# Optimization experiments

Hardware: AMD Instinct MI355X
Metric: run time of the kernel (lower is better)

The kernel has to match this reference:

```python
import jax, jax.numpy as jnp
import numpy as np
import math

B, L, H, NH = 8, 512, 512, 8
DH = H // NH


def setup_inputs() -> dict:
    key = jax.random.key(0)
    ks = jax.random.split(key, 12)
    src = jax.random.normal(ks[0], (B, L, H), dtype=jnp.float32)
    seq_len = jax.random.randint(ks[1], (B,), L // 2, L + 1).astype(jnp.int32)
    seq_len = seq_len.at[0].set(L)  # guarantee max(seq_len) == L
    pe = jax.random.normal(ks[2], (2 * L, H), dtype=jnp.float32) * 0.02
    s = 1.0 / math.sqrt(H)
    Wq = jax.random.normal(ks[3], (H, H), dtype=jnp.float32) * s
    bq = jnp.zeros((H,), jnp.float32)
    Wk = jax.random.normal(ks[4], (H, H), dtype=jnp.float32) * s
    bk = jnp.zeros((H,), jnp.float32)
    Wv = jax.random.normal(ks[5], (H, H), dtype=jnp.float32) * s
    bv = jnp.zeros((H,), jnp.float32)
    Wr = jax.random.normal(ks[6], (H, H), dtype=jnp.float32) * s
    br = jnp.zeros((H,), jnp.float32)
    u = jax.random.normal(ks[7], (NH, DH), dtype=jnp.float32) * 0.02
    v = jax.random.normal(ks[8], (NH, DH), dtype=jnp.float32) * 0.02
    gamma = jnp.ones((H,), jnp.float32)
    beta = jnp.zeros((H,), jnp.float32)
    return dict(src=src, seq_len=seq_len, pe=pe, Wq=Wq, bq=bq, Wk=Wk, bk=bk,
                Wv=Wv, bv=bv, Wr=Wr, br=br, u=u, v=v, gamma=gamma, beta=beta)


def reference(src, seq_len, pe, Wq, bq, Wk, bk, Wv, bv, Wr, br, u, v, gamma, beta):
    b, l, h = src.shape
    dh = h // NH
    # relative distance rel[i,j] = j - i, lookup pe[rel + L]  -> [L, L, H]
    rel = jnp.arange(l)[None, :] - jnp.arange(l)[:, None]
    R = pe[rel + l]
    # projections (torch Linear: y = x W^T + b)
    q = src @ Wq.T + bq
    k = src @ Wk.T + bk
    val = src @ Wv.T + bv
    R = R @ Wr.T + br
    # split heads
    q = q.reshape(b, l, NH, dh)
    k = k.reshape(b, l, NH, dh)
    val = val.reshape(b, l, NH, dh)
    R = R.reshape(l, l, NH, dh)
    # Transformer-XL score terms
    A = jnp.einsum('bihd,bjhd->bhij', q, k)
    Bt = jnp.einsum('bihd,ijhd->bhij', q, R)
    C = jnp.einsum('hd,bjhd->bhj', u, k)[:, :, None, :]
    D = jnp.einsum('ijhd,hd->hij', R, v)[None]
    scores = (A + Bt + C + D) / math.sqrt(dh)
    # key-side padding mask
    mask = jnp.arange(l)[None, :] < seq_len[:, None]  # [B, L]
    scores = jnp.where(mask[:, None, None, :], scores, jnp.float32(-1e15))
    attn = jax.nn.softmax(scores, axis=-1)
    out = jnp.einsum('bhij,bjhd->bihd', attn, val).reshape(b, l, h)
    res = src + out
    # LayerNorm (eps=1e-5) then exact GELU
    mu = jnp.mean(res, axis=-1, keepdims=True)
    var = jnp.mean((res - mu) ** 2, axis=-1, keepdims=True)
    ln = (res - mu) * jax.lax.rsqrt(var + 1e-5) * gamma + beta
    return jax.nn.gelu(ln, approximate=False)
```

## Files before the change

### kernel.cpp

```cpp
#include <hip/hip_runtime.h>
#include <math.h>

#define Bn 8
#define Ln 512
#define Hn 512
#define NHn 8
#define DHn 64

typedef __attribute__((ext_vector_type(8))) short short8;
typedef __attribute__((ext_vector_type(4))) float f32x4;

__device__ __forceinline__ unsigned short f2bf(float f) {
    unsigned int u = __float_as_uint(f);
    unsigned int r = (u + 0x7FFFu + ((u >> 16) & 1u)) >> 16;
    return (unsigned short)r;
}
__device__ __forceinline__ float bf2f(unsigned short s) {
    return __uint_as_float(((unsigned int)s) << 16);
}

__global__ __launch_bounds__(256) void convert_kernel(
    const float* __restrict__ src, const float* __restrict__ pe,
    const float* __restrict__ Wq, const float* __restrict__ Wk,
    const float* __restrict__ Wv, const float* __restrict__ Wr,
    const float* __restrict__ bq, const float* __restrict__ bk,
    const float* __restrict__ bv,
    unsigned short* __restrict__ src_bf, unsigned short* __restrict__ pe_bf,
    unsigned short* __restrict__ Wcat_bf, unsigned short* __restrict__ Wr_bf,
    float* __restrict__ bcat)
{
    const int bid = blockIdx.x;
    const int tid = threadIdx.x;
    const float* in; unsigned short* outp; int base4;
    if (bid < 2048)      { in = src; outp = src_bf;           base4 = bid; }
    else if (bid < 2560) { in = pe;  outp = pe_bf;            base4 = bid - 2048; }
    else if (bid < 2816) { in = Wq;  outp = Wcat_bf;          base4 = bid - 2560; }
    else if (bid < 3072) { in = Wk;  outp = Wcat_bf + 262144; base4 = bid - 2816; }
    else if (bid < 3328) { in = Wv;  outp = Wcat_bf + 524288; base4 = bid - 3072; }
    else if (bid < 3584) { in = Wr;  outp = Wr_bf;            base4 = bid - 3328; }
    else {
        const int idx = (bid - 3584) * 256 + tid;
        if (idx < 512)            bcat[idx] = bq[idx];
        else if (idx < 1024)      bcat[idx] = bk[idx - 512];
        else if (idx < 1536)      bcat[idx] = bv[idx - 1024];
        return;
    }
    const int i4 = (base4 * 256 + tid) * 4;
    float4 x = *(const float4*)&in[i4];
    ushort4 o;
    o.x = f2bf(x.x); o.y = f2bf(x.y); o.z = f2bf(x.z); o.w = f2bf(x.w);
    *(ushort4*)&outp[i4] = o;
}

__global__ __launch_bounds__(256) void gemm_kernel(
    const unsigned short* __restrict__ src_bf,
    const unsigned short* __restrict__ Wcat_bf,
    const unsigned short* __restrict__ pe_bf,
    const unsigned short* __restrict__ Wr_bf,
    const float* __restrict__ bcat, const float* __restrict__ br,
    unsigned short* __restrict__ QKb,
    unsigned short* __restrict__ VTg,
    unsigned short* __restrict__ Rpb)
{
    const int bid = blockIdx.x;
    int mode, m0, n0;
    const unsigned short *A, *B;
    if (bid < 256) {
        mode = 0; n0 = (bid & 7) * 128; m0 = (bid >> 3) * 128;
        A = src_bf + (size_t)m0 * 512;
        B = Wcat_bf + (size_t)n0 * 512;
    } else if (bid < 384) {
        mode = 1; m0 = ((bid - 256) & 3) * 128; n0 = ((bid - 256) >> 2) * 128;
        A = Wcat_bf + (size_t)(1024 + m0) * 512;
        B = src_bf + (size_t)n0 * 512;
    } else {
        mode = 2; n0 = ((bid - 384) & 3) * 128; m0 = ((bid - 384) >> 2) * 128;
        A = pe_bf + (size_t)m0 * 512;
        B = Wr_bf + (size_t)n0 * 512;
    }

    __shared__ unsigned short As[128 * 32];
    __shared__ unsigned short Bs[128 * 32];

    const int t = threadIdx.x;
    const int wave = t >> 6, lane = t & 63;
    const int wm = (wave >> 1) * 64;
    const int wn = (wave & 1) * 64;

    f32x4 acc[4][4] = {};

    const int srow = wave * 32 + (lane >> 2);
    const int scol = (lane & 3) * 8;
    const unsigned short* Ag = A + (size_t)srow * 512 + scol;
    const unsigned short* Bg = B + (size_t)srow * 512 + scol;
    unsigned short* AsW = &As[srow * 32 + scol];
    unsigned short* BsW = &Bs[srow * 32 + scol];

    uint4 a0 = *(const uint4*)(Ag);
    uint4 a1 = *(const uint4*)(Ag + 16 * 512);
    uint4 b0 = *(const uint4*)(Bg);
    uint4 b1 = *(const uint4*)(Bg + 16 * 512);

    for (int k0 = 0; k0 < 512; k0 += 32) {
        __syncthreads();
        *(uint4*)(AsW)           = a0;
        *(uint4*)(AsW + 16 * 32) = a1;
        *(uint4*)(BsW)           = b0;
        *(uint4*)(BsW + 16 * 32) = b1;
        __syncthreads();

        if (k0 + 32 < 512) {
            a0 = *(const uint4*)(Ag + k0 + 32);
            a1 = *(const uint4*)(Ag + k0 + 32 + 16 * 512);
            b0 = *(const uint4*)(Bg + k0 + 32);
            b1 = *(const uint4*)(Bg + k0 + 32 + 16 * 512);
        }

        short8 af[4], bf[4];
        #pragma unroll
        for (int mt = 0; mt < 4; ++mt)
            af[mt] = *(const short8*)&As[(wm + mt * 16 + (lane & 15)) * 32 + (lane >> 4) * 8];
        #pragma unroll
        for (int nt = 0; nt < 4; ++nt)
            bf[nt] = *(const short8*)&Bs[(wn + nt * 16 + (lane & 15)) * 32 + (lane >> 4) * 8];
        #pragma unroll
        for (int mt = 0; mt < 4; ++mt)
            #pragma unroll
            for (int nt = 0; nt < 4; ++nt)
                acc[mt][nt] = __builtin_amdgcn_mfma_f32_16x16x32_bf16(
                    af[mt], bf[nt], acc[mt][nt], 0, 0, 0);
    }

    const int crow = (lane >> 4) * 4;
    const int ccol = lane & 15;
    if (mode == 0) {
        #pragma unroll
        for (int mt = 0; mt < 4; ++mt)
            #pragma unroll
            for (int nt = 0; nt < 4; ++nt) {
                const int n = n0 + wn + nt * 16 + ccol;
                const float bn = bcat[n];
                #pragma unroll
                for (int r = 0; r < 4; ++r) {
                    const int m = m0 + wm + mt * 16 + crow + r;
                    QKb[(size_t)m * 1024 + n] = f2bf(acc[mt][nt][r] + bn);
                }
            }
    } else if (mode == 1) {
        #pragma unroll
        for (int mt = 0; mt < 4; ++mt)
            #pragma unroll
            for (int nt = 0; nt < 4; ++nt) {
                const int n = n0 + wn + nt * 16 + ccol;
                #pragma unroll
                for (int r = 0; r < 4; ++r) {
                    const int dv = m0 + wm + mt * 16 + crow + r;
                    VTg[(size_t)dv * 4096 + n] = f2bf(acc[mt][nt][r] + bcat[1024 + dv]);
                }
            }
    } else {
        #pragma unroll
        for (int mt = 0; mt < 4; ++mt)
            #pragma unroll
            for (int nt = 0; nt < 4; ++nt) {
                const int n = n0 + wn + nt * 16 + ccol;
                const float bn = br[n];
                #pragma unroll
                for (int r = 0; r < 4; ++r) {
                    const int m = m0 + wm + mt * 16 + crow + r;
                    Rpb[(size_t)m * 512 + n] = f2bf(acc[mt][nt][r] + bn);
                }
            }
    }
}

#define PADK 72
__global__ __launch_bounds__(256) void attn_kernel(
    const unsigned short* __restrict__ QKb,
    const unsigned short* __restrict__ VTg,
    const unsigned short* __restrict__ Rpb,
    const float* __restrict__ u, const float* __restrict__ v,
    const int* __restrict__ seq_len, unsigned short* __restrict__ Ob)
{
    const int i0 = blockIdx.x * 64;
    const int h  = blockIdx.y;
    const int b  = blockIdx.z;
    const int slen = seq_len[b];
    const int njt = (slen + 63) >> 6;

    __shared__ unsigned short k_s [64 * PADK];
    __shared__ unsigned short vT_s[64 * PADK];
    __shared__ unsigned short rs_s[64 * PADK];
    __shared__ unsigned short p_s [64 * PADK];
    __shared__ unsigned short qrTT[128 * 72];

    const int t = threadIdx.x;
    const int wave = t >> 6, lane = t & 63;
    const int l = lane & 15, g = lane >> 4;

    short8 af_qu[2], af_qv[2];
    {
        const unsigned short* qrow =
            QKb + (size_t)(b * 512 + i0 + wave * 16 + l) * 1024 + h * 64;
        #pragma unroll
        for (int kk = 0; kk < 2; ++kk) {
            const int c = kk * 32 + g * 8;
            unsigned short q8[8];
            *(uint4*)q8 = *(const uint4*)(qrow + c);
            float4 u0 = *(const float4*)(u + h * 64 + c);
            float4 u1 = *(const float4*)(u + h * 64 + c + 4);
            float4 v0 = *(const float4*)(v + h * 64 + c);
            float4 v1 = *(const float4*)(v + h * 64 + c + 4);
            float uf[8] = {u0.x,u0.y,u0.z,u0.w,u1.x,u1.y,u1.z,u1.w};
            float vf[8] = {v0.x,v0.y,v0.z,v0.w,v1.x,v1.y,v1.z,v1.w};
            short8 qu, qv;
            #pragma unroll
            for (int e = 0; e < 8; ++e) {
                float qf = bf2f(q8[e]);
                qu[e] = (short)f2bf(qf + uf[e]);
                qv[e] = (short)f2bf(qf + vf[e]);
            }
            af_qu[kk] = qu; af_qv[kk] = qv;
        }
    }

    float m_run[4], l_run[4];
    f32x4 accO[4] = {};
    #pragma unroll
    for (int r = 0; r < 4; ++r) { m_run[r] = -3.0e38f; l_run[r] = 0.f; }

    const int jr = t >> 2, c0 = (t & 3) * 16;

    auto btChunk = [&](int slot0) {
        #pragma unroll
        for (int nt8 = 0; nt8 < 4; ++nt8) {
            f32x4 a = {};
            #pragma unroll
            for (int kk = 0; kk < 2; ++kk) {
                short8 br8 = *(const short8*)&rs_s[(nt8 * 16 + l) * PADK + kk * 32 + g * 8];
                a = __builtin_amdgcn_mfma_f32_16x16x32_bf16(af_qv[kk], br8, a, 0, 0, 0);
            }
            const int sl = slot0 + nt8 * 16 + l;
            ushort4 w4;
            w4.x = f2bf(a[0]); w4.y = f2bf(a[1]); w4.z = f2bf(a[2]); w4.w = f2bf(a[3]);
            *(ushort4*)(qrTT + sl * 72 + wave * 16 + g * 4) = w4;
        }
    };

    const unsigned short* rpA = Rpb + (size_t)(448 - i0 + jr) * 512 + h * 64 + c0;
    uint4 rA0 = *(const uint4*)(rpA);
    uint4 rA1 = *(const uint4*)(rpA + 8);
    const unsigned short* kp0 = QKb + (size_t)(b * 512 + jr) * 1024 + 512 + h * 64 + c0;
    uint4 kc0 = *(const uint4*)(kp0), kc1 = *(const uint4*)(kp0 + 8);
    const unsigned short* vp0 = VTg + (size_t)(h * 64 + jr) * 4096 + b * 512 + c0;
    uint4 vc0 = *(const uint4*)(vp0), vc1 = *(const uint4*)(vp0 + 8);
    const unsigned short* rp0 = Rpb + (size_t)(512 - i0 + jr) * 512 + h * 64 + c0;
    uint4 rc0 = *(const uint4*)(rp0), rc1 = *(const uint4*)(rp0 + 8);

    *(uint4*)(rs_s + jr * PADK + c0)     = rA0;
    *(uint4*)(rs_s + jr * PADK + c0 + 8) = rA1;
    __syncthreads();
    btChunk((448 - i0) & 127);

    for (int jt = 0; jt < njt; ++jt) {
        const int j0 = jt * 64;
        __syncthreads();

        *(uint4*)(k_s  + jr * PADK + c0)     = kc0;
        *(uint4*)(k_s  + jr * PADK + c0 + 8) = kc1;
        *(uint4*)(vT_s + jr * PADK + c0)     = vc0;
        *(uint4*)(vT_s + jr * PADK + c0 + 8) = vc1;
        *(uint4*)(rs_s + jr * PADK + c0)     = rc0;
        *(uint4*)(rs_s + jr * PADK + c0 + 8) = rc1;
        __syncthreads();

        if (jt + 1 < njt) {
            const unsigned short* kp =
                QKb + (size_t)(b * 512 + j0 + 64 + jr) * 1024 + 512 + h * 64 + c0;
            kc0 = *(const uint4*)(kp); kc1 = *(const uint4*)(kp + 8);
            const unsigned short* vp =
                VTg + (size_t)(h * 64 + jr) * 4096 + b * 512 + j0 + 64 + c0;
            vc0 = *(const uint4*)(vp); vc1 = *(const uint4*)(vp + 8);
            const unsigned short* rp =
                Rpb + (size_t)(j0 + 64 - i0 + 512 + jr) * 512 + h * 64 + c0;
            rc0 = *(const uint4*)(rp); rc1 = *(const uint4*)(rp + 8);
        }

        btChunk((j0 - i0 + 512) & 127);

        f32x4 accA[4];
        #pragma unroll
        for (int nt = 0; nt < 4; ++nt) {
            f32x4 a = {};
            #pragma unroll
            for (int kk = 0; kk < 2; ++kk) {
                short8 bk8 = *(const short8*)&k_s[(nt * 16 + l) * PADK + kk * 32 + g * 8];
                a = __builtin_amdgcn_mfma_f32_16x16x32_bf16(af_qu[kk], bk8, a, 0, 0, 0);
            }
            accA[nt] = a;
        }

        float sv[4][4];
        #pragma unroll
        for (int nt = 0; nt < 4; ++nt)
            #pragma unroll
            for (int r = 0; r < 4; ++r) {
                const int il = wave * 16 + g * 4 + r;
                const int slot = (j0 + nt * 16 + l - i0 - il + 512) & 127;
                const float qr = bf2f(qrTT[slot * 72 + il]);
                float s = (accA[nt][r] + qr) * 0.125f;
                if (j0 + nt * 16 + l >= slen) s = -1e15f;
                sv[nt][r] = s;
            }

        float alpha_r[4];
        #pragma unroll
        for (int r = 0; r < 4; ++r) {
            float tm = fmaxf(fmaxf(sv[0][r], sv[1][r]), fmaxf(sv[2][r], sv[3][r]));
            tm = fmaxf(tm, __shfl_xor(tm, 1, 64));
            tm = fmaxf(tm, __shfl_xor(tm, 2, 64));
            tm = fmaxf(tm, __shfl_xor(tm, 4, 64));
            tm = fmaxf(tm, __shfl_xor(tm, 8, 64));
            const float mn = fmaxf(m_run[r], tm);
            alpha_r[r] = __expf(m_run[r] - mn);
            m_run[r] = mn;
            float ss = 0.f;
            #pragma unroll
            for (int nt = 0; nt < 4; ++nt) {
                const float pe_ = __expf(sv[nt][r] - mn);
                sv[nt][r] = pe_; ss += pe_;
            }
            ss += __shfl_xor(ss, 1, 64);
            ss += __shfl_xor(ss, 2, 64);
            ss += __shfl_xor(ss, 4, 64);
            ss += __shfl_xor(ss, 8, 64);
            l_run[r] = l_run[r] * alpha_r[r] + ss;
        }

        #pragma unroll
        for (int nt = 0; nt < 4; ++nt)
            #pragma unroll
            for (int r = 0; r < 4; ++r)
                p_s[(wave * 16 + g * 4 + r) * PADK + nt * 16 + l] = f2bf(sv[nt][r]);

        #pragma unroll
        for (int nt = 0; nt < 4; ++nt)
            #pragma unroll
            for (int r = 0; r < 4; ++r)
                accO[nt][r] *= alpha_r[r];

        short8 pa[2];
        #pragma unroll
        for (int kk = 0; kk < 2; ++kk)
            pa[kk] = *(const short8*)&p_s[(wave * 16 + l) * PADK + kk * 32 + g * 8];
        #pragma unroll
        for (int nt = 0; nt < 4; ++nt) {
            #pragma unroll
            for (int kk = 0; kk < 2; ++kk) {
                short8 bv8 = *(const short8*)&vT_s[(nt * 16 + l) * PADK + kk * 32 + g * 8];
                accO[nt] = __builtin_amdgcn_mfma_f32_16x16x32_bf16(pa[kk], bv8, accO[nt], 0, 0, 0);
            }
        }
    }

    float inv[4];
    #pragma unroll
    for (int r = 0; r < 4; ++r) inv[r] = 1.0f / l_run[r];
    #pragma unroll
    for (int nt = 0; nt < 4; ++nt)
        #pragma unroll
        for (int r = 0; r < 4; ++r)
            Ob[(size_t)(b * 512 + i0 + wave * 16 + g * 4 + r) * 512 + h * 64 + nt * 16 + l]
                = f2bf(accO[nt][r] * inv[r]);
}

__global__ __launch_bounds__(256) void ln_gelu_kernel(
    const float* __restrict__ src, const unsigned short* __restrict__ Ob,
    const float* __restrict__ gamma, const float* __restrict__ beta,
    float* __restrict__ out)
{
    const int row  = blockIdx.x * 4 + (threadIdx.x >> 6);
    const int lane = threadIdx.x & 63;
    const int c0   = lane * 8;
    const float* s = &src[(size_t)row * 512 + c0];
    float4 s0 = *(const float4*)(s);
    float4 s1 = *(const float4*)(s + 4);
    unsigned short o8[8];
    *(uint4*)o8 = *(const uint4*)(Ob + (size_t)row * 512 + c0);
    float x[8];
    x[0] = s0.x + bf2f(o8[0]); x[1] = s0.y + bf2f(o8[1]);
    x[2] = s0.z + bf2f(o8[2]); x[3] = s0.w + bf2f(o8[3]);
    x[4] = s1.x + bf2f(o8[4]); x[5] = s1.y + bf2f(o8[5]);
    x[6] = s1.z + bf2f(o8[6]); x[7] = s1.w + bf2f(o8[7]);
    float sum = 0.f;
    #pragma unroll
    for (int e = 0; e < 8; ++e) sum += x[e];
    #pragma unroll
    for (int off = 32; off >= 1; off >>= 1) sum += __shfl_xor(sum, off, 64);
    const float mean = sum * (1.0f / 512.0f);
    float var = 0.f;
    #pragma unroll
    for (int e = 0; e < 8; ++e) { float d = x[e] - mean; var += d * d; }
    #pragma unroll
    for (int off = 32; off >= 1; off >>= 1) var += __shfl_xor(var, off, 64);
    var *= (1.0f / 512.0f);
    const float inv = rsqrtf(var + 1e-5f);
    float4 g0 = *(const float4*)(gamma + c0);
    float4 g1 = *(const float4*)(gamma + c0 + 4);
    float4 b0 = *(const float4*)(beta + c0);
    float4 b1 = *(const float4*)(beta + c0 + 4);
    float gm[8] = {g0.x,g0.y,g0.z,g0.w,g1.x,g1.y,g1.z,g1.w};
    float bt[8] = {b0.x,b0.y,b0.z,b0.w,b1.x,b1.y,b1.z,b1.w};
    float r8[8];
    #pragma unroll
    for (int e = 0; e < 8; ++e) {
        float ln = (x[e] - mean) * inv * gm[e] + bt[e];
        r8[e] = 0.5f * ln * (1.0f + erff(ln * 0.70710678118654752f));
    }
    float* op = &out[(size_t)row * 512 + c0];
    *(float4*)(op)     = make_float4(r8[0], r8[1], r8[2], r8[3]);
    *(float4*)(op + 4) = make_float4(r8[4], r8[5], r8[6], r8[7]);
}

extern "C" void kernel_launch(void* const* d_in, const int* in_sizes, int n_in,
                              void* d_out, int out_size, void* d_ws, size_t ws_size,
                              hipStream_t stream)
{
    const float* src     = (const float*)d_in[0];
    const int*   seq_len = (const int*)  d_in[1];
    const float* pe      = (const float*)d_in[2];
    const float* Wq      = (const float*)d_in[3];
    const float* bq      = (const float*)d_in[4];
    const float* Wk      = (const float*)d_in[5];
    const float* bk      = (const float*)d_in[6];
    const float* Wv      = (const float*)d_in[7];
    const float* bv      = (const float*)d_in[8];
    const float* Wr      = (const float*)d_in[9];
    const float* br      = (const float*)d_in[10];
    const float* u       = (const float*)d_in[11];
    const float* v       = (const float*)d_in[12];
    const float* gamma   = (const float*)d_in[13];
    const float* beta    = (const float*)d_in[14];
    float* out = (float*)d_out;

    char* w = (char*)d_ws;
    unsigned short* QKb     = (unsigned short*)(w);
    unsigned short* VTg     = (unsigned short*)(w + 8388608);
    unsigned short* Rpb     = (unsigned short*)(w + 12582912);
    unsigned short* Ob      = (unsigned short*)(w + 13631488);
    unsigned short* src_bf  = (unsigned short*)(w + 17825792);
    unsigned short* pe_bf   = (unsigned short*)(w + 22020096);
    unsigned short* Wcat_bf = (unsigned short*)(w + 23068672);
    unsigned short* Wr_bf   = (unsigned short*)(w + 24641536);
    float*          bcat    = (float*)         (w + 25165824);

    convert_kernel<<<dim3(3590), 256, 0, stream>>>(
        src, pe, Wq, Wk, Wv, Wr, bq, bk, bv,
        src_bf, pe_bf, Wcat_bf, Wr_bf, bcat);

    gemm_kernel<<<dim3(416), 256, 0, stream>>>(
        src_bf, Wcat_bf, pe_bf, Wr_bf, bcat, br, QKb, VTg, Rpb);

    attn_kernel<<<dim3(8, NHn, Bn), 256, 0, stream>>>(QKb, VTg, Rpb, u, v, seq_len, Ob);

    ln_gelu_kernel<<<dim3(Bn * Ln / 4), 256, 0, stream>>>(src, Ob, gamma, beta, out);
}
```

Measured before the change: 133.6 us.

## Double GEMM K-tile to 64 and pad LDS rows to cut bank conflicts

```diff
diff --git a/kernel.cpp b/kernel.cpp
--- a/kernel.cpp
+++ b/kernel.cpp
@@ -52,6 +52,7 @@
     *(ushort4*)&outp[i4] = o;
 }
 
+#define GSTR 72
 __global__ __launch_bounds__(256) void gemm_kernel(
     const unsigned short* __restrict__ src_bf,
     const unsigned short* __restrict__ Wcat_bf,
@@ -79,60 +80,77 @@
         B = Wr_bf + (size_t)n0 * 512;
     }
 
-    __shared__ unsigned short As[128 * 32];
-    __shared__ unsigned short Bs[128 * 32];
+    __shared__ unsigned short As[128 * GSTR];
+    __shared__ unsigned short Bs[128 * GSTR];
 
     const int t = threadIdx.x;
     const int wave = t >> 6, lane = t & 63;
     const int wm = (wave >> 1) * 64;
     const int wn = (wave & 1) * 64;
+    const int l = lane & 15, g = lane >> 4;
 
     f32x4 acc[4][4] = {};
 
     const int srow = wave * 32 + (lane >> 2);
-    const int scol = (lane & 3) * 8;
+    const int scol = (lane & 3) * 16;
     const unsigned short* Ag = A + (size_t)srow * 512 + scol;
     const unsigned short* Bg = B + (size_t)srow * 512 + scol;
-    unsigned short* AsW = &As[srow * 32 + scol];
-    unsigned short* BsW = &Bs[srow * 32 + scol];
+    unsigned short* AsW = &As[srow * GSTR + scol];
+    unsigned short* BsW = &Bs[srow * GSTR + scol];
 
     uint4 a0 = *(const uint4*)(Ag);
-    uint4 a1 = *(const uint4*)(Ag + 16 * 512);
+    uint4 a1 = *(const uint4*)(Ag + 8);
+    uint4 a2 = *(const uint4*)(Ag + 16 * 512);
+    uint4 a3 = *(const uint4*)(Ag + 16 * 512 + 8);
     uint4 b0 = *(const uint4*)(Bg);
-    uint4 b1 = *(const uint4*)(Bg + 16 * 512);
-
-    for (int k0 = 0; k0 < 512; k0 += 32) {
+    uint4 b1 = *(const uint4*)(Bg + 8);
+    uint4 b2 = *(const uint4*)(Bg + 16 * 512);
+    uint4 b3 = *(const uint4*)(Bg + 16 * 512 + 8);
+
+    for (int k0 = 0; k0 < 512; k0 += 64) {
         __syncthreads();
-        *(uint4*)(AsW)           = a0;
-        *(uint4*)(AsW + 16 * 32) = a1;
-        *(uint4*)(BsW)           = b0;
-        *(uint4*)(BsW + 16 * 32) = b1;
+        *(uint4*)(AsW)                = a0;
+        *(uint4*)(AsW + 8)            = a1;
+        *(uint4*)(AsW + 16 * GSTR)    = a2;
+        *(uint4*)(AsW + 16 * GSTR + 8) = a3;
+        *(uint4*)(BsW)                = b0;
+        *(uint4*)(BsW + 8)            = b1;
+        *(uint4*)(BsW + 16 * GSTR)    = b2;
+        *(uint4*)(BsW + 16 * GSTR + 8) = b3;
         __syncthreads();
 
-        if (k0 + 32 < 512) {
-            a0 = *(const uint4*)(Ag + k0 + 32);
-            a1 = *(const uint4*)(Ag + k0 + 32 + 16 * 512);
-            b0 = *(const uint4*)(Bg + k0 + 32);
-            b1 = *(const uint4*)(Bg + k0 + 32 + 16 * 512);
-        }
-
-        short8 af[4], bf[4];
-        #pragma unroll
-        for (int mt = 0; mt < 4; ++mt)
-            af[mt] = *(const short8*)&As[(wm + mt * 16 + (lane & 15)) * 32 + (lane >> 4) * 8];
-        #pragma unroll
-        for (int nt = 0; nt < 4; ++nt)
-            bf[nt] = *(const short8*)&Bs[(wn + nt * 16 + (lane & 15)) * 32 + (lane >> 4) * 8];
-        #pragma unroll
-        for (int mt = 0; mt < 4; ++mt)
+        if (k0 + 64 < 512) {
+            const int kn = k0 + 64;
+            a0 = *(const uint4*)(Ag + kn);
+            a1 = *(const uint4*)(Ag + kn + 8);
+            a2 = *(const uint4*)(Ag + kn + 16 * 512);
+            a3 = *(const uint4*)(Ag + kn + 16 * 512 + 8);
+            b0 = *(const uint4*)(Bg + kn);
+            b1 = *(const uint4*)(Bg + kn + 8);
+            b2 = *(const uint4*)(Bg + kn + 16 * 512);
+            b3 = *(const uint4*)(Bg + kn + 16 * 512 + 8);
+        }
+
+        #pragma unroll
+        for (int kk = 0; kk < 2; ++kk) {
+            short8 af[4], bf[4];
+            #pragma unroll
+            for (int mt = 0; mt < 4; ++mt)
+                af[mt] = *(const short8*)&As[(wm + mt * 16 + l) * GSTR + kk * 32 + g * 8];
             #pragma unroll
             for (int nt = 0; nt < 4; ++nt)
-                acc[mt][nt] = __builtin_amdgcn_mfma_f32_16x16x32_bf16(
-                    af[mt], bf[nt], acc[mt][nt], 0, 0, 0);
-    }
-
-    const int crow = (lane >> 4) * 4;
-    const int ccol = lane & 15;
+                bf[nt] = *(const short8*)&Bs[(wn + nt * 16 + l) * GSTR + kk * 32 + g * 8];
+            #pragma unroll
+            for (int mt = 0; mt < 4; ++mt)
+                #pragma unroll
+                for (int nt = 0; nt < 4; ++nt)
+                    acc[mt][nt] = __builtin_amdgcn_mfma_f32_16x16x32_bf16(
+                        af[mt], bf[nt], acc[mt][nt], 0, 0, 0);
+        }
+    }
+
+    const int crow = g * 4;
+    const int ccol = l;
     if (mode == 0) {
         #pragma unroll
         for (int mt = 0; mt < 4; ++mt)
```

New measurement: 133.3 us. About the same (-0.3%).
